# Performance work log

Measured on AMD Instinct MI355X. Metric: run time of the kernel, lower is better.

## Reference

```python
import jax, jax.numpy as jnp
import numpy as np

T, B, Y, H, R, L = 256, 1024, 32, 1024, 512, 2  # seq_len, batch, y_dim, h_dim, rnn_dim, n_layers


def setup_inputs() -> dict:
    key = jax.random.key(0)
    ks = jax.random.split(key, 18)
    s = jnp.float32(0.05)

    def w(k, shape):
        return jax.random.normal(k, shape, dtype=jnp.float32) * s

    return {
        "y": jax.random.normal(ks[0], (T, B, Y), dtype=jnp.float32),
        # decoder MLP: Linear(R->H), ReLU, Linear(H->H), ReLU
        "dec_w1": w(ks[1], (H, R)), "dec_b1": jnp.zeros((H,), jnp.float32),
        "dec_w2": w(ks[2], (H, H)), "dec_b2": jnp.zeros((H,), jnp.float32),
        # dec_mean: Linear(H->Y); dec_std: Linear(H->Y) + Softplus
        "mean_w": w(ks[3], (Y, H)), "mean_b": jnp.zeros((Y,), jnp.float32),
        "std_w": w(ks[4], (Y, H)), "std_b": jnp.zeros((Y,), jnp.float32),
        # 2-layer GRU, torch gate order (r, z, n)
        "gru_wih0": w(ks[5], (3 * R, Y)), "gru_whh0": w(ks[6], (3 * R, R)),
        "gru_bih0": jnp.zeros((3 * R,), jnp.float32), "gru_bhh0": jnp.zeros((3 * R,), jnp.float32),
        "gru_wih1": w(ks[7], (3 * R, R)), "gru_whh1": w(ks[8], (3 * R, R)),
        "gru_bih1": jnp.zeros((3 * R,), jnp.float32), "gru_bhh1": jnp.zeros((3 * R,), jnp.float32),
    }


def _gru_cell(x, h, wih, whh, bih, bhh):
    # torch GRUCell math, gates ordered (r, z, n)
    gi = x @ wih.T + bih          # [B, 3R]
    gh = h @ whh.T + bhh          # [B, 3R]
    ir, iz, inn = jnp.split(gi, 3, axis=-1)
    hr, hz, hn = jnp.split(gh, 3, axis=-1)
    r = jax.nn.sigmoid(ir + hr)
    z = jax.nn.sigmoid(iz + hz)
    n = jnp.tanh(inn + r * hn)
    return (1.0 - z) * n + z * h


def reference(y, dec_w1, dec_b1, dec_w2, dec_b2, mean_w, mean_b, std_w, std_b,
              gru_wih0, gru_whh0, gru_bih0, gru_bhh0,
              gru_wih1, gru_whh1, gru_bih1, gru_bhh1):
    log2pi = jnp.float32(np.log(2.0 * np.pi))
    batch = y.shape[1]
    h0 = jnp.zeros((L, batch, R), dtype=y.dtype)

    def step(carry, y_t):
        h, nll = carry
        # decode from top-layer hidden state (before the GRU update)
        d = jax.nn.relu(h[-1] @ dec_w1.T + dec_b1)
        d = jax.nn.relu(d @ dec_w2.T + dec_b2)
        mean_t = d @ mean_w.T + mean_b
        std_t = jax.nn.softplus(d @ std_w.T + std_b)
        # nll_gauss: 0.5 * sum((x-mu)^2/std^2 + 2*log(std) + log(2*pi))
        nll_t = 0.5 * jnp.sum((y_t - mean_t) ** 2 / (std_t ** 2)
                              + 2.0 * jnp.log(std_t) + log2pi)
        # single GRU step (2 layers)
        h_l0 = _gru_cell(y_t, h[0], gru_wih0, gru_whh0, gru_bih0, gru_bhh0)
        h_l1 = _gru_cell(h_l0, h[1], gru_wih1, gru_whh1, gru_bih1, gru_bhh1)
        return (jnp.stack([h_l0, h_l1]), nll + nll_t), None

    (_, nll), _ = jax.lax.scan(step, (h0, jnp.float32(0.0)), y)
    return nll
```

## Files before the change

### kernel.cpp

```cpp
#include <hip/hip_runtime.h>
#include <math.h>

#define TT   256
#define BB   1024
#define YDIM 32
#define HDIM 1024
#define RDIM 512

typedef __attribute__((ext_vector_type(8))) short frag8;
typedef __attribute__((ext_vector_type(4))) float f32x4;

#define LDS_BUF 16384

#define OFF_NLL   ((size_t)0)
#define OFF_HAF   ((size_t)4096)
#define SZ_HF     ((size_t)BB*RDIM*4)
#define OFF_HBF   (OFF_HAF + 2*SZ_HF)
#define OFF_HA16  (OFF_HBF + 2*SZ_HF)
#define SZ_H16    ((size_t)BB*RDIM*2)
#define OFF_HB16  (OFF_HA16 + 2*SZ_H16)
#define OFF_D1    (OFF_HB16 + 2*SZ_H16)
#define SZ_DBUF   ((size_t)BB*HDIM*2)
#define OFF_D2    (OFF_D1 + 2*SZ_DBUF)
#define OFF_Y16   (OFF_D2 + 2*SZ_DBUF)
#define OFF_WG0I  (OFF_Y16 + (size_t)TT*BB*YDIM*2)
#define OFF_WG0H  (OFF_WG0I + (size_t)1536*YDIM*2)
#define OFF_WG1I  (OFF_WG0H + (size_t)1536*RDIM*2)
#define OFF_WG1H  (OFF_WG1I + (size_t)1536*RDIM*2)
#define OFF_WD1   (OFF_WG1H + (size_t)1536*RDIM*2)
#define OFF_WD2   (OFF_WD1 + (size_t)HDIM*RDIM*2)
#define OFF_WMS   (OFF_WD2 + (size_t)HDIM*HDIM*2)
#define OFF_BI0   (OFF_WMS + (size_t)64*HDIM*2)
#define OFF_BH0   (OFF_BI0 + 1536*4)
#define OFF_BI1   (OFF_BH0 + 1536*4)
#define OFF_BH1   (OFF_BI1 + 1536*4)

__device__ __forceinline__ short f2bf(float f) {
  union { float f; unsigned u; } v; v.f = f;
  unsigned r = (v.u + 0x7fffu + ((v.u >> 16) & 1u)) >> 16;
  return (short)r;
}
__device__ __forceinline__ void cvt8(const float* s, short* d) {
  float4 a = *(const float4*)s;
  float4 b = *(const float4*)(s + 4);
  frag8 v;
  v[0]=f2bf(a.x); v[1]=f2bf(a.y); v[2]=f2bf(a.z); v[3]=f2bf(a.w);
  v[4]=f2bf(b.x); v[5]=f2bf(b.y); v[6]=f2bf(b.z); v[7]=f2bf(b.w);
  *(frag8*)d = v;
}
__device__ __forceinline__ int permRow(int n) {
  int q = n / 48, r = n - 48 * q, g = r >> 4, u = r & 15;
  return g * 512 + q * 16 + u;
}
__device__ __forceinline__ float sigf(float x) { return 1.0f / (1.0f + expf(-x)); }

__device__ __forceinline__ void gload16(const short* g, short* l) {
  __builtin_amdgcn_global_load_lds(
      (const __attribute__((address_space(1))) void*)g,
      (__attribute__((address_space(3))) void*)l, 16, 0, 0);
}

template<int N> __device__ __forceinline__ void waitv() {
  if constexpr (N == 0)      asm volatile("s_waitcnt vmcnt(0)" ::: "memory");
  else if constexpr (N == 6) asm volatile("s_waitcnt vmcnt(6)" ::: "memory");
  else if constexpr (N == 7) asm volatile("s_waitcnt vmcnt(7)" ::: "memory");
  else if constexpr (N == 8) asm volatile("s_waitcnt vmcnt(8)" ::: "memory");
  else                       asm volatile("s_waitcnt vmcnt(0)" ::: "memory");
}

template<int MF, int NF, int NROWSB>
__device__ __forceinline__ void kloop64(
    const short* __restrict__ A, int lda, int m0,
    const short* __restrict__ B, int ldb, int K,
    int wm, int wn, short* lds, f32x4 (*acc)[NF], int tid)
{
  const int l = tid & 63, w = tid >> 6, u = l & 15, quad = l >> 4;
  const int nk = K >> 6;
  constexpr int BUNITS = NROWSB << 3;
  constexpr int LPS = 4 + NROWSB / 32;

  auto stage = [&](int kc, int buf) {
    short* base = lds + buf * LDS_BUF;
    const int k0 = kc << 6;
    for (int c = (w << 6); c < 1024; c += 256) {
      int p = c + l, r = p >> 3, q = (p & 7) ^ (r & 7);
      gload16(A + (size_t)(m0 + r) * lda + k0 + (q << 3), base + (c << 3));
    }
    short* bb = base + 8192;
    for (int c = (w << 6); c < BUNITS; c += 256) {
      int p = c + l, r = p >> 3, q = (p & 7) ^ (r & 7);
      gload16(B + (size_t)r * ldb + k0 + (q << 3), bb + (c << 3));
    }
  };

  stage(0, 0);
  for (int kc = 0; kc < nk; ++kc) {
    asm volatile("s_waitcnt lgkmcnt(0)" ::: "memory");
    __builtin_amdgcn_s_barrier();
    if (kc + 1 < nk) {
      stage(kc + 1, (kc + 1) & 1);
      waitv<LPS>();
    } else {
      waitv<0>();
    }
    __builtin_amdgcn_s_barrier();
    asm volatile("" ::: "memory");
    const short* base = lds + (kc & 1) * LDS_BUF;
#pragma unroll
    for (int kk2 = 0; kk2 < 2; ++kk2) {
      const int q = (kk2 << 2) + quad;
      const int aoff = (q ^ (u & 7)) << 3;
      frag8 a[MF], b[NF];
#pragma unroll
      for (int i = 0; i < MF; ++i)
        a[i] = *(const frag8*)(base + ((wm + (i << 4) + u) << 6) + aoff);
#pragma unroll
      for (int f = 0; f < NF; ++f)
        b[f] = *(const frag8*)(base + 8192 + ((wn + (f << 4) + u) << 6) + aoff);
#pragma unroll
      for (int i = 0; i < MF; ++i)
#pragma unroll
        for (int f = 0; f < NF; ++f)
          acc[i][f] = __builtin_amdgcn_mfma_f32_16x16x32_bf16(a[i], b[f], acc[i][f], 0, 0, 0);
    }
  }
}

template<int MF, int NF>
__device__ __forceinline__ void kloop32(
    const short* __restrict__ A, int lda, int m0,
    const short* __restrict__ B, int nrowsB,
    int wm, int wn, short* lds, f32x4 (*acc)[NF], int tid)
{
  const int l = tid & 63, w = tid >> 6, u = l & 15, quad = l >> 4;
  short* base = lds;
  for (int c = (w << 6); c < 512; c += 256) {
    int p = c + l, r = p >> 2, q = (p & 3) ^ (r & 3);
    gload16(A + (size_t)(m0 + r) * lda + (q << 3), base + (c << 3));
  }
  short* bb = base + 4096;
  const int bunits = nrowsB << 2;
  for (int c = (w << 6); c < bunits; c += 256) {
    int p = c + l, r = p >> 2, q = (p & 3) ^ (r & 3);
    gload16(B + (size_t)r * 32 + (q << 3), bb + (c << 3));
  }
  __syncthreads();
  const int aoff = (quad ^ (u & 3)) << 3;
  frag8 a[MF], b[NF];
#pragma unroll
  for (int i = 0; i < MF; ++i)
    a[i] = *(const frag8*)(base + ((wm + (i << 4) + u) << 5) + aoff);
#pragma unroll
  for (int f = 0; f < NF; ++f)
    b[f] = *(const frag8*)(base + 4096 + ((wn + (f << 4) + u) << 5) + aoff);
#pragma unroll
  for (int i = 0; i < MF; ++i)
#pragma unroll
    for (int f = 0; f < NF; ++f)
      acc[i][f] = __builtin_amdgcn_mfma_f32_16x16x32_bf16(a[i], b[f], acc[i][f], 0, 0, 0);
  __syncthreads();
}

template<bool GI32>
__device__ void gru_tile(int mb, int nb,
                         const short* Ax, int ldx, const short* Wgi,
                         const short* Ah, const short* Wgh,
                         const float* bi, const float* bh,
                         const float* hold, float* hout, short* h16out,
                         short* lds, int tid)
{
  f32x4 zero = {0.f, 0.f, 0.f, 0.f};
  f32x4 gi[4][3], gh[4][3];
#pragma unroll
  for (int i = 0; i < 4; ++i)
#pragma unroll
    for (int f = 0; f < 3; ++f) { gi[i][f] = zero; gh[i][f] = zero; }
  const int w = tid >> 6, l = tid & 63, u = l & 15, quad = l >> 4;
  const int wm = (w & 1) * 64, wn = (w >> 1) * 48;
  if (GI32)
    kloop32<4, 3>(Ax, ldx, mb * 128, Wgi, 96, wm, wn, lds, gi, tid);
  else
    kloop64<4, 3, 96>(Ax, ldx, mb * 128, Wgi, RDIM, RDIM, wm, wn, lds, gi, tid);
  kloop64<4, 3, 96>(Ah, RDIM, mb * 128, Wgh, RDIM, RDIM, wm, wn, lds, gh, tid);

  const int np = nb * 96 + (w >> 1) * 48 + u;
  const float bir = bi[np], biz = bi[np + 16], bin = bi[np + 32];
  const float bhr = bh[np], bhz = bh[np + 16], bhn = bh[np + 32];
  const int unit = nb * 32 + (w >> 1) * 16 + u;
#pragma unroll
  for (int i = 0; i < 4; ++i)
#pragma unroll
    for (int j = 0; j < 4; ++j) {
      int row = mb * 128 + wm + 16 * i + quad * 4 + j;
      float r = sigf((gi[i][0][j] + bir) + (gh[i][0][j] + bhr));
      float z = sigf((gi[i][1][j] + biz) + (gh[i][1][j] + bhz));
      float n = tanhf((gi[i][2][j] + bin) + r * (gh[i][2][j] + bhn));
      float ho = hold[(size_t)row * RDIM + unit];
      float hn = (1.f - z) * n + z * ho;
      hout[(size_t)row * RDIM + unit] = hn;
      h16out[(size_t)row * RDIM + unit] = f2bf(hn);
    }
}

__device__ void dec_tile(int mb, int nb, const short* A, int lda, int K,
                         const short* W, const float* bias, short* outp,
                         short* lds, int tid)
{
  f32x4 zero = {0.f, 0.f, 0.f, 0.f};
  f32x4 acc[4][4];
#pragma unroll
  for (int i = 0; i < 4; ++i)
#pragma unroll
    for (int f = 0; f < 4; ++f) acc[i][f] = zero;
  const int w = tid >> 6, l = tid & 63, u = l & 15, quad = l >> 4;
  const int wm = (w & 1) * 64, wn = (w >> 1) * 64;
  kloop64<4, 4, 128>(A, lda, mb * 128, W, K, K, wm, wn, lds, acc, tid);
  const int colb = nb * 128 + wn + u;
  float bv[4];
#pragma unroll
  for (int f = 0; f < 4; ++f) bv[f] = bias[colb + 16 * f];
#pragma unroll
  for (int i = 0; i < 4; ++i)
#pragma unroll
    for (int f = 0; f < 4; ++f)
#pragma unroll
      for (int j = 0; j < 4; ++j) {
        int row = mb * 128 + wm + 16 * i + quad * 4 + j;
        float v = acc[i][f][j] + bv[f];
        if (v < 0.f) v = 0.f;
        outp[(size_t)row * HDIM + colb + 16 * f] = f2bf(v);
      }
}

__device__ void ms_tile(int mb, int tstep, const short* d2p, const short* Wms,
                        const float* mbias, const float* sbias, const float* y,
                        float* nll, short* lds, int tid)
{
  f32x4 zero = {0.f, 0.f, 0.f, 0.f};
  f32x4 acc[2][4];
#pragma unroll
  for (int i = 0; i < 2; ++i)
#pragma unroll
    for (int f = 0; f < 4; ++f) acc[i][f] = zero;
  const int w = tid >> 6, l = tid & 63, u = l & 15, quad = l >> 4;
  kloop64<2, 4, 64>(d2p, HDIM, mb * 128, Wms, HDIM, HDIM, w * 32, 0, lds, acc, tid);
  float lsum = 0.f;
#pragma unroll
  for (int i = 0; i < 2; ++i)
#pragma unroll
    for (int j = 0; j < 4; ++j) {
      int row = mb * 128 + w * 32 + 16 * i + quad * 4 + j;
      const float* yr = y + ((size_t)tstep * BB + row) * YDIM;
#pragma unroll
      for (int f = 0; f < 2; ++f) {
        int c = 16 * f + u;
        float m  = acc[i][f][j] + mbias[c];
        float sp = acc[i][f + 2][j] + sbias[c];
        float sg = (sp > 20.f) ? sp : log1pf(expf(sp));
        float dv = (yr[c] - m) / sg;
        lsum += dv * dv + 2.f * logf(sg) + 1.8378770664093453f;
      }
    }
  lsum *= 0.5f;
#pragma unroll
  for (int o = 32; o; o >>= 1) lsum += __shfl_xor(lsum, o);
  if (l == 0) atomicAdd(nll, lsum);
}

__global__ __launch_bounds__(256) void prepack_kernel(
    const float* y, const float* dw1, const float* dw2,
    const float* mw, const float* sw,
    const float* wih0, const float* whh0, const float* bih0, const float* bhh0,
    const float* wih1, const float* whh1, const float* bih1, const float* bhh1,
    char* __restrict__ ws)
{
  const size_t g = (size_t)blockIdx.x * 256 + threadIdx.x;
  const size_t N = (size_t)gridDim.x * 256;
  float4 z4 = {0.f, 0.f, 0.f, 0.f};
  float4* hz = (float4*)(ws + OFF_HAF);
  for (size_t i = g; i < (size_t)4 * BB * RDIM / 4; i += N) hz[i] = z4;
  int4 zi = {0, 0, 0, 0};
  int4* h16z = (int4*)(ws + OFF_HA16);
  for (size_t i = g; i < (size_t)4 * BB * RDIM / 8; i += N) h16z[i] = zi;
  if (g == 0) *(float*)(ws + OFF_NLL) = 0.f;

  short* y16  = (short*)(ws + OFF_Y16);
  short* Wg0i = (short*)(ws + OFF_WG0I);
  short* Wg0h = (short*)(ws + OFF_WG0H);
  short* Wg1i = (short*)(ws + OFF_WG1I);
  short* Wg1h = (short*)(ws + OFF_WG1H);
  short* Wd1  = (short*)(ws + OFF_WD1);
  short* Wd2  = (short*)(ws + OFF_WD2);
  short* Wms  = (short*)(ws + OFF_WMS);
  float* bi0  = (float*)(ws + OFF_BI0);
  float* bh0  = (float*)(ws + OFF_BH0);
  float* bi1  = (float*)(ws + OFF_BI1);
  float* bh1  = (float*)(ws + OFF_BH1);

  for (size_t s = g; s < (size_t)TT * BB * YDIM / 8; s += N)
    cvt8(y + s * 8, y16 + s * 8);
  for (size_t s = g; s < (size_t)1536 * RDIM / 8; s += N) {
    int row = (int)(s >> 6), seg = (int)(s & 63) << 3;
    int pr = permRow(row);
    cvt8(whh0 + (size_t)pr * RDIM + seg, Wg0h + (size_t)row * RDIM + seg);
    cvt8(wih1 + (size_t)pr * RDIM + seg, Wg1i + (size_t)row * RDIM + seg);
    cvt8(whh1 + (size_t)pr * RDIM + seg, Wg1h + (size_t)row * RDIM + seg);
  }
  for (size_t s = g; s < (size_t)1536 * YDIM / 8; s += N) {
    int row = (int)(s >> 2), seg = (int)(s & 3) << 3;
    cvt8(wih0 + (size_t)permRow(row) * YDIM + seg, Wg0i + (size_t)row * YDIM + seg);
  }
  for (size_t s = g; s < (size_t)HDIM * RDIM / 8; s += N)
    cvt8(dw1 + s * 8, Wd1 + s * 8);
  for (size_t s = g; s < (size_t)HDIM * HDIM / 8; s += N)
    cvt8(dw2 + s * 8, Wd2 + s * 8);
  for (size_t s = g; s < (size_t)64 * HDIM / 8; s += N) {
    int row = (int)(s >> 7), seg = (int)(s & 127) << 3;
    const float* src = (row < 32) ? (mw + (size_t)row * HDIM + seg)
                                  : (sw + (size_t)(row - 32) * HDIM + seg);
    cvt8(src, Wms + (size_t)row * HDIM + seg);
  }
  for (size_t s = g; s < 1536; s += N) {
    int pr = permRow((int)s);
    bi0[s] = bih0[pr]; bh0[s] = bhh0[pr];
    bi1[s] = bih1[pr]; bh1[s] = bhh1[pr];
  }
}

__global__ __launch_bounds__(256, 2) void phase_kernel(
    int p, const float* __restrict__ y,
    const float* db1, const float* db2, const float* mbias, const float* sbias,
    char* __restrict__ ws)
{
  __shared__ short lds[2 * LDS_BUF];
  const int tid = threadIdx.x;
  const int t = blockIdx.x;
  const int cur = p & 1, prv = cur ^ 1;

  float* hAf = (float*)(ws + OFF_HAF);
  float* hBf = (float*)(ws + OFF_HBF);
  short* hA16 = (short*)(ws + OFF_HA16);
  short* hB16 = (short*)(ws + OFF_HB16);
  short* d10 = (short*)(ws + OFF_D1);
  short* d20 = (short*)(ws + OFF_D2);
  const short* y16 = (const short*)(ws + OFF_Y16);

  float* hAfc = hAf + (size_t)cur * BB * RDIM;
  float* hAfp = hAf + (size_t)prv * BB * RDIM;
  float* hBfc = hBf + (size_t)cur * BB * RDIM;
  float* hBfp = hBf + (size_t)prv * BB * RDIM;
  short* hA16c = hA16 + (size_t)cur * BB * RDIM;
  short* hA16p = hA16 + (size_t)prv * BB * RDIM;
  short* hB16c = hB16 + (size_t)cur * BB * RDIM;
  short* hB16p = hB16 + (size_t)prv * BB * RDIM;
  short* d1c = d10 + (size_t)cur * BB * HDIM;
  short* d1p = d10 + (size_t)prv * BB * HDIM;
  short* d2c = d20 + (size_t)cur * BB * HDIM;
  short* d2p = d20 + (size_t)prv * BB * HDIM;

  const short* Wg0i = (const short*)(ws + OFF_WG0I);
  const short* Wg0h = (const short*)(ws + OFF_WG0H);
  const short* Wg1i = (const short*)(ws + OFF_WG1I);
  const short* Wg1h = (const short*)(ws + OFF_WG1H);
  const short* Wd1  = (const short*)(ws + OFF_WD1);
  const short* Wd2  = (const short*)(ws + OFF_WD2);
  const short* Wms  = (const short*)(ws + OFF_WMS);
  const float* bi0  = (const float*)(ws + OFF_BI0);
  const float* bh0  = (const float*)(ws + OFF_BH0);
  const float* bi1  = (const float*)(ws + OFF_BI1);
  const float* bh1  = (const float*)(ws + OFF_BH1);
  float* nllp = (float*)(ws + OFF_NLL);

  if (t < 128) {
    if (p >= 1 && p <= 255) {
      int mb = t >> 4, nb = t & 15;
      gru_tile<false>(mb, nb,
                      hA16p, RDIM, Wg1i + (size_t)nb * 96 * RDIM,
                      hB16p, Wg1h + (size_t)nb * 96 * RDIM,
                      bi1, bh1, hBfp, hBfc, hB16c, lds, tid);
    }
  } else if (t < 192) {
    if (p >= 2 && p <= 257) {
      int q = t - 128, mb = q >> 3, nb = q & 7;
      dec_tile(mb, nb, d1p, HDIM, HDIM, Wd2 + (size_t)nb * 128 * HDIM,
               db2, d2c, lds, tid);
    }
  } else if (t < 200) {
    if (p >= 3 && p <= 258) {
      ms_tile(t - 192, p - 3, d2p, Wms, mbias, sbias, y, nllp, lds, tid);
    }
  } else if (t < 328) {
    if (p <= 255) {
      int q = t - 200, mb = q >> 4, nb = q & 15;
      gru_tile<true>(mb, nb,
                     y16 + (size_t)p * BB * YDIM, YDIM, Wg0i + (size_t)nb * 96 * YDIM,
                     hA16p, Wg0h + (size_t)nb * 96 * RDIM,
                     bi0, bh0, hAfp, hAfc, hA16c, lds, tid);
    }
  } else {
    if (p >= 1 && p <= 256) {
      int q = t - 328, mb = q >> 3, nb = q & 7;
      dec_tile(mb, nb, hB16p, RDIM, RDIM, Wd1 + (size_t)nb * 128 * RDIM,
               db1, d1c, lds, tid);
    }
  }
}

__global__ void finish_kernel(float* out, const char* ws)
{
  if (threadIdx.x == 0 && blockIdx.x == 0)
    out[0] = *(const float*)(ws + OFF_NLL);
}

extern "C" void kernel_launch(void* const* d_in, const int* in_sizes, int n_in,
                              void* d_out, int out_size, void* d_ws, size_t ws_size,
                              hipStream_t stream) {
  (void)in_sizes; (void)n_in; (void)out_size; (void)ws_size;
  const float* y    = (const float*)d_in[0];
  const float* dw1  = (const float*)d_in[1];
  const float* db1  = (const float*)d_in[2];
  const float* dw2  = (const float*)d_in[3];
  const float* db2  = (const float*)d_in[4];
  const float* mw   = (const float*)d_in[5];
  const float* mbias= (const float*)d_in[6];
  const float* sw   = (const float*)d_in[7];
  const float* sbias= (const float*)d_in[8];
  const float* wih0 = (const float*)d_in[9];
  const float* whh0 = (const float*)d_in[10];
  const float* bih0 = (const float*)d_in[11];
  const float* bhh0 = (const float*)d_in[12];
  const float* wih1 = (const float*)d_in[13];
  const float* whh1 = (const float*)d_in[14];
  const float* bih1 = (const float*)d_in[15];
  const float* bhh1 = (const float*)d_in[16];
  char* ws = (char*)d_ws;
  float* out = (float*)d_out;

  prepack_kernel<<<256, 256, 0, stream>>>(y, dw1, dw2, mw, sw,
                                          wih0, whh0, bih0, bhh0,
                                          wih1, whh1, bih1, bhh1, ws);
  for (int p = 0; p < 259; ++p)
    phase_kernel<<<392, 256, 0, stream>>>(p, y, db1, db2, mbias, sbias, ws);
  finish_kernel<<<1, 1, 0, stream>>>(out, ws);
}
```

Before: 5.370 ms.

## Fuse both GRU layer tiles per block and shrink grid to fit one block per CU

```diff
diff --git a/kernel.cpp b/kernel.cpp
--- a/kernel.cpp
+++ b/kernel.cpp
@@ -11,6 +11,7 @@
 typedef __attribute__((ext_vector_type(4))) float f32x4;
 
 #define LDS_BUF 16384
+#define DBUF    10240
 
 #define OFF_NLL   ((size_t)0)
 #define OFF_HAF   ((size_t)4096)
@@ -62,6 +63,7 @@
 
 template<int N> __device__ __forceinline__ void waitv() {
   if constexpr (N == 0)      asm volatile("s_waitcnt vmcnt(0)" ::: "memory");
+  else if constexpr (N == 5) asm volatile("s_waitcnt vmcnt(5)" ::: "memory");
   else if constexpr (N == 6) asm volatile("s_waitcnt vmcnt(6)" ::: "memory");
   else if constexpr (N == 7) asm volatile("s_waitcnt vmcnt(7)" ::: "memory");
   else if constexpr (N == 8) asm volatile("s_waitcnt vmcnt(8)" ::: "memory");
@@ -127,6 +129,63 @@
 }
 
 template<int MF, int NF>
+__device__ __forceinline__ void kloopd32(
+    const short* __restrict__ A, int lda, int m0,
+    const short* __restrict__ B1, const short* __restrict__ B2,
+    int wm, int wn, short* lds, f32x4 (*acc1)[NF], f32x4 (*acc2)[NF], int tid)
+{
+  const int l = tid & 63, w = tid >> 6, u = l & 15, quad = l >> 4;
+
+  auto stage = [&](int kc, int buf) {
+    short* base = lds + buf * DBUF;
+    const int k0 = kc << 5;
+    for (int c = (w << 6); c < 512; c += 256) {
+      int p = c + l, r = p >> 2, q = (p & 3) ^ (r & 3);
+      gload16(A + (size_t)(m0 + r) * lda + k0 + (q << 3), base + (c << 3));
+    }
+    short* bb = base + 4096;
+    for (int c = (w << 6); c < 768; c += 256) {
+      int p = c + l, r = p >> 2, q = (p & 3) ^ (r & 3);
+      const short* src = (r < 96) ? (B1 + (size_t)r * RDIM)
+                                  : (B2 + (size_t)(r - 96) * RDIM);
+      gload16(src + k0 + (q << 3), bb + (c << 3));
+    }
+  };
+
+  stage(0, 0);
+  for (int kc = 0; kc < 16; ++kc) {
+    asm volatile("s_waitcnt lgkmcnt(0)" ::: "memory");
+    __builtin_amdgcn_s_barrier();
+    if (kc + 1 < 16) {
+      stage(kc + 1, (kc + 1) & 1);
+      waitv<5>();
+    } else {
+      waitv<0>();
+    }
+    __builtin_amdgcn_s_barrier();
+    asm volatile("" ::: "memory");
+    const short* base = lds + (kc & 1) * DBUF;
+    const int aoff = (quad ^ (u & 3)) << 3;
+    frag8 a[MF], b1[NF], b2[NF];
+#pragma unroll
+    for (int i = 0; i < MF; ++i)
+      a[i] = *(const frag8*)(base + ((wm + (i << 4) + u) << 5) + aoff);
+#pragma unroll
+    for (int f = 0; f < NF; ++f) {
+      b1[f] = *(const frag8*)(base + 4096 + ((wn + (f << 4) + u) << 5) + aoff);
+      b2[f] = *(const frag8*)(base + 7168 + ((wn + (f << 4) + u) << 5) + aoff);
+    }
+#pragma unroll
+    for (int i = 0; i < MF; ++i)
+#pragma unroll
+      for (int f = 0; f < NF; ++f) {
+        acc1[i][f] = __builtin_amdgcn_mfma_f32_16x16x32_bf16(a[i], b1[f], acc1[i][f], 0, 0, 0);
+        acc2[i][f] = __builtin_amdgcn_mfma_f32_16x16x32_bf16(a[i], b2[f], acc2[i][f], 0, 0, 0);
+      }
+  }
+}
+
+template<int MF, int NF>
 __device__ __forceinline__ void kloop32(
     const short* __restrict__ A, int lda, int m0,
     const short* __restrict__ B, int nrowsB,
@@ -161,45 +220,70 @@
   __syncthreads();
 }
 
-template<bool GI32>
-__device__ void gru_tile(int mb, int nb,
-                         const short* Ax, int ldx, const short* Wgi,
-                         const short* Ah, const short* Wgh,
-                         const float* bi, const float* bh,
-                         const float* hold, float* hout, short* h16out,
-                         short* lds, int tid)
+__device__ void gruf_tile(int p, int mb, int nb,
+                          const short* y16p, const short* hA16p, const short* hB16p,
+                          const short* Wg0i, const short* Wg0h,
+                          const short* Wg1i, const short* Wg1h,
+                          const float* bi0, const float* bh0,
+                          const float* bi1, const float* bh1,
+                          const float* hAfp, float* hAfc, short* hA16c,
+                          const float* hBfp, float* hBfc, short* hB16c,
+                          short* lds, int tid)
 {
   f32x4 zero = {0.f, 0.f, 0.f, 0.f};
-  f32x4 gi[4][3], gh[4][3];
+  f32x4 gi0[4][3], gh0[4][3], gi1[4][3], gh1[4][3];
 #pragma unroll
   for (int i = 0; i < 4; ++i)
 #pragma unroll
-    for (int f = 0; f < 3; ++f) { gi[i][f] = zero; gh[i][f] = zero; }
+    for (int f = 0; f < 3; ++f) { gi0[i][f] = zero; gh0[i][f] = zero;
+                                  gi1[i][f] = zero; gh1[i][f] = zero; }
   const int w = tid >> 6, l = tid & 63, u = l & 15, quad = l >> 4;
   const int wm = (w & 1) * 64, wn = (w >> 1) * 48;
-  if (GI32)
-    kloop32<4, 3>(Ax, ldx, mb * 128, Wgi, 96, wm, wn, lds, gi, tid);
-  else
-    kloop64<4, 3, 96>(Ax, ldx, mb * 128, Wgi, RDIM, RDIM, wm, wn, lds, gi, tid);
-  kloop64<4, 3, 96>(Ah, RDIM, mb * 128, Wgh, RDIM, RDIM, wm, wn, lds, gh, tid);
+
+  kloop32<4, 3>(y16p, YDIM, mb * 128, Wg0i + (size_t)nb * 96 * YDIM, 96, wm, wn, lds, gi0, tid);
+  kloopd32<4, 3>(hA16p, RDIM, mb * 128,
+                 Wg1i + (size_t)nb * 96 * RDIM, Wg0h + (size_t)nb * 96 * RDIM,
+                 wm, wn, lds, gi1, gh0, tid);
+  __syncthreads();
+  kloop64<4, 3, 96>(hB16p, RDIM, mb * 128, Wg1h + (size_t)nb * 96 * RDIM,
+                    RDIM, RDIM, wm, wn, lds, gh1, tid);
 
   const int np = nb * 96 + (w >> 1) * 48 + u;
-  const float bir = bi[np], biz = bi[np + 16], bin = bi[np + 32];
-  const float bhr = bh[np], bhz = bh[np + 16], bhn = bh[np + 32];
   const int unit = nb * 32 + (w >> 1) * 16 + u;
-#pragma unroll
-  for (int i = 0; i < 4; ++i)
-#pragma unroll
-    for (int j = 0; j < 4; ++j) {
-      int row = mb * 128 + wm + 16 * i + quad * 4 + j;
-      float r = sigf((gi[i][0][j] + bir) + (gh[i][0][j] + bhr));
-      float z = sigf((gi[i][1][j] + biz) + (gh[i][1][j] + bhz));
-      float n = tanhf((gi[i][2][j] + bin) + r * (gh[i][2][j] + bhn));
-      float ho = hold[(size_t)row * RDIM + unit];
-      float hn = (1.f - z) * n + z * ho;
-      hout[(size_t)row * RDIM + unit] = hn;
-      h16out[(size_t)row * RDIM + unit] = f2bf(hn);
-    }
+  {
+    const float bir = bi0[np], biz = bi0[np + 16], bin = bi0[np + 32];
+    const float bhr = bh0[np], bhz = bh0[np + 16], bhn = bh0[np + 32];
+#pragma unroll
+    for (int i = 0; i < 4; ++i)
+#pragma unroll
+      for (int j = 0; j < 4; ++j) {
+        int row = mb * 128 + wm + 16 * i + quad * 4 + j;
+        float r = sigf((gi0[i][0][j] + bir) + (gh0[i][0][j] + bhr));
+        float z = sigf((gi0[i][1][j] + biz) + (gh0[i][1][j] + bhz));
+        float n = tanhf((gi0[i][2][j] + bin) + r * (gh0[i][2][j] + bhn));
+        float ho = hAfp[(size_t)row * RDIM + unit];
+        float hn = (1.f - z) * n + z * ho;
+        hAfc[(size_t)row * RDIM + unit] = hn;
+        hA16c[(size_t)row * RDIM + unit] = f2bf(hn);
+      }
+  }
+  if (p >= 1) {
+    const float bir = bi1[np], biz = bi1[np + 16], bin = bi1[np + 32];
+    const float bhr = bh1[np], bhz = bh1[np + 16], bhn = bh1[np + 32];
+#pragma unroll
+    for (int i = 0; i < 4; ++i)
+#pragma unroll
+      for (int j = 0; j < 4; ++j) {
+        int row = mb * 128 + wm + 16 * i + quad * 4 + j;
+        float r = sigf((gi1[i][0][j] + bir) + (gh1[i][0][j] + bhr));
+        float z = sigf((gi1[i][1][j] + biz) + (gh1[i][1][j] + bhz));
+        float n = tanhf((gi1[i][2][j] + bin) + r * (gh1[i][2][j] + bhn));
+        float ho = hBfp[(size_t)row * RDIM + unit];
+        float hn = (1.f - z) * n + z * ho;
+        hBfc[(size_t)row * RDIM + unit] = hn;
+        hB16c[(size_t)row * RDIM + unit] = f2bf(hn);
+      }
+  }
 }
 
 __device__ void dec_tile(int mb, int nb, const short* A, int lda, int K,
@@ -327,7 +411,7 @@
   }
 }
 
-__global__ __launch_bounds__(256, 2) void phase_kernel(
+__global__ __launch_bounds__(256, 1) void phase_kernel(
     int p, const float* __restrict__ y,
     const float* db1, const float* db2, const float* mbias, const float* sbias,
     char* __restrict__ ws)
@@ -372,12 +456,14 @@
   float* nllp = (float*)(ws + OFF_NLL);
 
   if (t < 128) {
-    if (p >= 1 && p <= 255) {
+    if (p <= 255) {
       int mb = t >> 4, nb = t & 15;
-      gru_tile<false>(mb, nb,
-                      hA16p, RDIM, Wg1i + (size_t)nb * 96 * RDIM,
-                      hB16p, Wg1h + (size_t)nb * 96 * RDIM,
-                      bi1, bh1, hBfp, hBfc, hB16c, lds, tid);
+      gruf_tile(p, mb, nb,
+                y16 + (size_t)p * BB * YDIM, hA16p, hB16p,
+                Wg0i, Wg0h, Wg1i, Wg1h,
+                bi0, bh0, bi1, bh1,
+                hAfp, hAfc, hA16c,
+                hBfp, hBfc, hB16c, lds, tid);
     }
   } else if (t < 192) {
     if (p >= 2 && p <= 257) {
@@ -385,23 +471,17 @@
       dec_tile(mb, nb, d1p, HDIM, HDIM, Wd2 + (size_t)nb * 128 * HDIM,
                db2, d2c, lds, tid);
     }
-  } else if (t < 200) {
-    if (p >= 3 && p <= 258) {
-      ms_tile(t - 192, p - 3, d2p, Wms, mbias, sbias, y, nllp, lds, tid);
-    }
-  } else if (t < 328) {
-    if (p <= 255) {
-      int q = t - 200, mb = q >> 4, nb = q & 15;
-      gru_tile<true>(mb, nb,
-                     y16 + (size_t)p * BB * YDIM, YDIM, Wg0i + (size_t)nb * 96 * YDIM,
-                     hA16p, Wg0h + (size_t)nb * 96 * RDIM,
-                     bi0, bh0, hAfp, hAfc, hA16c, lds, tid);
-    }
-  } else {
+  } else if (t < 224) {
     if (p >= 1 && p <= 256) {
-      int q = t - 328, mb = q >> 3, nb = q & 7;
+      int q = t - 192, mb = q >> 3, nb = q & 7;
       dec_tile(mb, nb, hB16p, RDIM, RDIM, Wd1 + (size_t)nb * 128 * RDIM,
                db1, d1c, lds, tid);
+      dec_tile(mb + 4, nb, hB16p, RDIM, RDIM, Wd1 + (size_t)nb * 128 * RDIM,
+               db1, d1c, lds, tid);
+    }
+  } else {
+    if (p >= 3 && p <= 258) {
+      ms_tile(t - 224, p - 3, d2p, Wms, mbias, sbias, y, nllp, lds, tid);
     }
   }
 }
@@ -440,6 +520,6 @@
                                           wih0, whh0, bih0, bhh0,
                                           wih1, whh1, bih1, bhh1, ws);
   for (int p = 0; p < 259; ++p)
-    phase_kernel<<<392, 256, 0, stream>>>(p, y, db1, db2, mbias, sbias, ws);
+    phase_kernel<<<232, 256, 0, stream>>>(p, y, db1, db2, mbias, sbias, ws);
   finish_kernel<<<1, 1, 0, stream>>>(out, ws);
 }
```

Result: slower. 8.876 ms (+65.3%).
